# Kernel tuning notes

Hardware: AMD Instinct MI355X
Metric: run time of the kernel (lower is better)

Reference implementation:

```python
import jax, jax.numpy as jnp
import numpy as np

N = 2048          # num nodes == in_channels (f1 = graphs[0].shape[0])
F_IN = 2048       # node feature dim
G1 = 10           # ChebConv out channels
E = 65536         # num edges (avg degree 32)
NUM_CLASSES = 10  # fc1 output


def setup_inputs() -> dict:
    key = jax.random.key(0)
    ks = jax.random.split(key, 6)
    x = jax.random.normal(ks[0], (N, F_IN), dtype=jnp.float32)
    edge_index = jax.random.randint(ks[1], (2, E), 0, N)
    # ChebConv weights: one [F_IN, G1] matrix per Chebyshev order (K=2), glorot-ish init
    s = float(1.0 / np.sqrt(F_IN))
    W0 = jax.random.uniform(ks[2], (F_IN, G1), jnp.float32, -s, s)
    W1 = jax.random.uniform(ks[3], (F_IN, G1), jnp.float32, -s, s)
    b = jnp.zeros((G1,), jnp.float32)
    sf = float(1.0 / np.sqrt(G1))
    Wf = jax.random.uniform(ks[4], (G1, NUM_CLASSES), jnp.float32, -sf, sf)
    bf = jax.random.uniform(ks[5], (NUM_CLASSES,), jnp.float32, -sf, sf)
    return {"x": x, "edge_index": edge_index, "W0": W0, "W1": W1, "b": b, "Wf": Wf, "bf": bf}


def _cheb_edge_weights(edge_index):
    # PyG ChebConv default: sym-normalized Laplacian scaled with lambda_max=2.0.
    # L_hat = 2*L/lambda_max - I = -D^{-1/2} A D^{-1/2}  (zero diagonal).
    row, col = edge_index[0], edge_index[1]
    deg = jax.ops.segment_sum(jnp.ones((E,), jnp.float32), row, num_segments=N)
    dis = jnp.where(deg > 0, jax.lax.rsqrt(jnp.maximum(deg, 1.0)), 0.0)
    return -dis[row] * dis[col]


def reference(x, edge_index, W0, W1, b, Wf, bf):
    row, col = edge_index[0], edge_index[1]
    w = _cheb_edge_weights(edge_index)
    # Tx_0 = x ; Tx_1 = L_hat @ x via gather (source=row) + scatter-add (target=col)
    Tx1 = jax.ops.segment_sum(w[:, None] * x[row], col, num_segments=N)  # [N, F_IN]
    h = x @ W0 + Tx1 @ W1 + b                                            # ChebConv, K=2
    h = jax.nn.relu(h)
    logits = h @ Wf + bf                                                 # fc1
    return jax.nn.log_softmax(logits, axis=1)
```

## Files before the change

### kernel.cpp

```cpp
#include <hip/hip_runtime.h>

#define N_NODES 2048
#define F_IN    2048
#define G1      10
#define NCLS    10
#define NEDGE   65536
#define JCHUNKS 64
#define JPER    32
#define HSLICES 128
#define ZSLICES 64

__device__ float g_p[JCHUNKS * 20 * N_NODES];
__device__ int   g_degp[HSLICES * N_NODES];
__device__ float g_dis[N_NODES];
__device__ float g_y[N_NODES * 20];
__device__ float g_zp[2 * ZSLICES * N_NODES * 5];
__device__ float g_z[N_NODES * G1];

__global__ __launch_bounds__(256) void k_gemm(const float* __restrict__ x,
                                              const float* __restrict__ W0,
                                              const float* __restrict__ W1,
                                              const int* __restrict__ ei) {
    __shared__ float sx[256 * 33];
    int jc      = blockIdx.x;
    int rowbase = blockIdx.y * 256;
    int j0      = jc * JPER;

    #pragma unroll
    for (int rep = 0; rep < 8; ++rep) {
        int idx = rep * 256 + threadIdx.x;
        int r = idx >> 3, c4 = idx & 7;
        float4 v = *(const float4*)(x + (size_t)(rowbase + r) * F_IN + j0 + c4 * 4);
        float* d = sx + r * 33 + c4 * 4;
        d[0] = v.x; d[1] = v.y; d[2] = v.z; d[3] = v.w;
    }
    __syncthreads();

    float acc[20];
    #pragma unroll
    for (int k = 0; k < 20; ++k) acc[k] = 0.f;

    const float* xr = sx + threadIdx.x * 33;
    #pragma unroll
    for (int j = 0; j < JPER; ++j) {
        float xu = xr[j];
        const float* w0r = W0 + (size_t)(j0 + j) * G1;
        const float* w1r = W1 + (size_t)(j0 + j) * G1;
        #pragma unroll
        for (int k = 0; k < G1; ++k) {
            acc[k]      += xu * w0r[k];
            acc[10 + k] += xu * w1r[k];
        }
    }
    int row = rowbase + threadIdx.x;
    #pragma unroll
    for (int k = 0; k < 20; ++k)
        g_p[((size_t)jc * 20 + k) * N_NODES + row] = acc[k];

    if (blockIdx.y < 4) {
        int hs = blockIdx.y * JCHUNKS + jc;
        hs = blockIdx.y * 64 + jc;
        hs = (blockIdx.y << 5) * 2 + jc;
        hs = blockIdx.y * 32 + (jc & 31);
        if (jc < 32) {
            int slice = blockIdx.y * 32 + jc;
            __syncthreads();
            int* h = (int*)sx;
            #pragma unroll
            for (int t = threadIdx.x; t < N_NODES; t += 256) h[t] = 0;
            __syncthreads();
            int base = slice * (NEDGE / HSLICES);
            #pragma unroll
            for (int u = 0; u < 2; ++u)
                atomicAdd(&h[ei[base + u * 256 + threadIdx.x]], 1);
            __syncthreads();
            #pragma unroll
            for (int t = threadIdx.x; t < N_NODES; t += 256)
                g_degp[slice * N_NODES + t] = h[t];
        }
    }
}

__global__ __launch_bounds__(256) void k_reduce() {
    int t   = blockIdx.x * 256 + threadIdx.x;
    int k   = t >> 11;
    int row = t & (N_NODES - 1);
    float s = 0.f;
    #pragma unroll 16
    for (int jc = 0; jc < JCHUNKS; ++jc)
        s += g_p[((size_t)jc * 20 + k) * N_NODES + row];
    g_y[row * 20 + k] = s;
    if (t < N_NODES) {
        int d = 0;
        #pragma unroll 16
        for (int sl = 0; sl < HSLICES; ++sl) d += g_degp[sl * N_NODES + t];
        g_dis[t] = (d > 0) ? rsqrtf((float)d) : 0.f;
    }
}

__global__ __launch_bounds__(256) void k_scatter(const int* __restrict__ ei) {
    __shared__ float zl[N_NODES * 5];
    int khalf  = blockIdx.x >> 6;
    int bslice = blockIdx.x & (ZSLICES - 1);
    float4* zl4 = (float4*)zl;
    #pragma unroll
    for (int t = threadIdx.x; t < N_NODES * 5 / 4; t += 256)
        zl4[t] = make_float4(0.f, 0.f, 0.f, 0.f);
    __syncthreads();
    int base = bslice * (NEDGE / ZSLICES);
    #pragma unroll
    for (int u = 0; u < NEDGE / ZSLICES / 256; ++u) {
        int e = base + u * 256 + threadIdx.x;
        int r = ei[e], c = ei[NEDGE + e];
        float w = -g_dis[r] * g_dis[c];
        const float* y1 = g_y + r * 20 + 10 + khalf * 5;
        float* zz = zl + c * 5;
        #pragma unroll
        for (int kk = 0; kk < 5; ++kk) atomicAdd(&zz[kk], w * y1[kk]);
    }
    __syncthreads();
    float4* dst = (float4*)(g_zp + ((size_t)khalf * ZSLICES + bslice) * (N_NODES * 5));
    #pragma unroll
    for (int t = threadIdx.x; t < N_NODES * 5 / 4; t += 256) dst[t] = zl4[t];
}

__global__ __launch_bounds__(256) void k_zred() {
    int t = blockIdx.x * 256 + threadIdx.x;
    int khalf = t / (N_NODES * 5);
    int rem   = t % (N_NODES * 5);
    float s = 0.f;
    #pragma unroll 16
    for (int sl = 0; sl < ZSLICES; ++sl)
        s += g_zp[((size_t)khalf * ZSLICES + sl) * (N_NODES * 5) + rem];
    int i = rem / 5, kk = rem - i * 5;
    g_z[i * 10 + khalf * 5 + kk] = s;
}

__global__ __launch_bounds__(256) void k_final(const float* __restrict__ b,
                                               const float* __restrict__ Wf,
                                               const float* __restrict__ bfv,
                                               float* __restrict__ out) {
    int i = blockIdx.x * 256 + threadIdx.x;
    float h[G1];
    #pragma unroll
    for (int k = 0; k < G1; ++k)
        h[k] = fmaxf(g_y[i * 20 + k] + g_z[i * 10 + k] + b[k], 0.f);
    float lo[NCLS];
    #pragma unroll
    for (int c = 0; c < NCLS; ++c) lo[c] = bfv[c];
    #pragma unroll
    for (int k = 0; k < G1; ++k) {
        float hk = h[k];
        #pragma unroll
        for (int c = 0; c < NCLS; ++c) lo[c] += hk * Wf[k * NCLS + c];
    }
    float m = lo[0];
    #pragma unroll
    for (int c = 1; c < NCLS; ++c) m = fmaxf(m, lo[c]);
    float s = 0.f;
    #pragma unroll
    for (int c = 0; c < NCLS; ++c) s += expf(lo[c] - m);
    float ls = logf(s);
    #pragma unroll
    for (int c = 0; c < NCLS; ++c) out[i * NCLS + c] = lo[c] - m - ls;
}

extern "C" void kernel_launch(void* const* d_in, const int* in_sizes, int n_in,
                              void* d_out, int out_size, void* d_ws, size_t ws_size,
                              hipStream_t stream) {
    const float* x   = (const float*)d_in[0];
    const int*   ei  = (const int*)d_in[1];
    const float* W0  = (const float*)d_in[2];
    const float* W1  = (const float*)d_in[3];
    const float* b   = (const float*)d_in[4];
    const float* Wf  = (const float*)d_in[5];
    const float* bfv = (const float*)d_in[6];
    float* out = (float*)d_out;

    k_gemm<<<dim3(JCHUNKS, N_NODES / 256), 256, 0, stream>>>(x, W0, W1, ei);
    k_reduce<<<(N_NODES * 20) / 256, 256, 0, stream>>>();
    k_scatter<<<2 * ZSLICES, 256, 0, stream>>>(ei);
    k_zred<<<(N_NODES * G1) / 256, 256, 0, stream>>>();
    k_final<<<N_NODES / 256, 256, 0, stream>>>(b, Wf, bfv, out);
}
```

Before: 111.5 us.

## Fuse all stages into one persistent kernel with software grid barriers

Merges the GEMM, partial reduction, degree count, edge scatter, z reduction and final softmax into a single kernel of 512 blocks separated by atomic grid barriers. The GEMM is retiled to 128 rows by 64 columns with half the block per weight matrix, and degrees are counted with global atomics instead of per-slice histograms. This removes per-launch overhead and intermediate degree partial buffers. It relies on all blocks being co-resident and adds barrier spin cost.

```diff
diff --git a/kernel.cpp b/kernel.cpp
--- a/kernel.cpp
+++ b/kernel.cpp
@@ -5,164 +5,181 @@
 #define G1      10
 #define NCLS    10
 #define NEDGE   65536
-#define JCHUNKS 64
-#define JPER    32
-#define HSLICES 128
-#define ZSLICES 64
+#define JC      32
+#define JPER    64
+#define ROWS    128
+#define ZS      64
+#define GRID    512
+#define BLK     256
 
-__device__ float g_p[JCHUNKS * 20 * N_NODES];
-__device__ int   g_degp[HSLICES * N_NODES];
-__device__ float g_dis[N_NODES];
+__device__ float g_p[JC * 20 * N_NODES];
+__device__ int   g_deg[N_NODES];
 __device__ float g_y[N_NODES * 20];
-__device__ float g_zp[2 * ZSLICES * N_NODES * 5];
+__device__ float g_zp[2 * ZS * N_NODES * 5];
 __device__ float g_z[N_NODES * G1];
 
-__global__ __launch_bounds__(256) void k_gemm(const float* __restrict__ x,
-                                              const float* __restrict__ W0,
-                                              const float* __restrict__ W1,
-                                              const int* __restrict__ ei) {
-    __shared__ float sx[256 * 33];
-    int jc      = blockIdx.x;
-    int rowbase = blockIdx.y * 256;
-    int j0      = jc * JPER;
+__device__ unsigned g_bar_count = 0;
+__device__ unsigned g_bar_gen   = 0;
 
-    #pragma unroll
-    for (int rep = 0; rep < 8; ++rep) {
-        int idx = rep * 256 + threadIdx.x;
-        int r = idx >> 3, c4 = idx & 7;
-        float4 v = *(const float4*)(x + (size_t)(rowbase + r) * F_IN + j0 + c4 * 4);
-        float* d = sx + r * 33 + c4 * 4;
-        d[0] = v.x; d[1] = v.y; d[2] = v.z; d[3] = v.w;
+__device__ __forceinline__ void grid_barrier() {
+    __syncthreads();
+    if (threadIdx.x == 0) {
+        __threadfence();
+        unsigned gen = __hip_atomic_load(&g_bar_gen, __ATOMIC_ACQUIRE,
+                                         __HIP_MEMORY_SCOPE_AGENT);
+        unsigned prev = __hip_atomic_fetch_add(&g_bar_count, 1u, __ATOMIC_ACQ_REL,
+                                               __HIP_MEMORY_SCOPE_AGENT);
+        if (prev == (unsigned)(gridDim.x - 1)) {
+            __hip_atomic_store(&g_bar_count, 0u, __ATOMIC_RELAXED,
+                               __HIP_MEMORY_SCOPE_AGENT);
+            __hip_atomic_fetch_add(&g_bar_gen, 1u, __ATOMIC_RELEASE,
+                                   __HIP_MEMORY_SCOPE_AGENT);
+        } else {
+            while (__hip_atomic_load(&g_bar_gen, __ATOMIC_ACQUIRE,
+                                     __HIP_MEMORY_SCOPE_AGENT) == gen)
+                __builtin_amdgcn_s_sleep(2);
+        }
     }
     __syncthreads();
+}
 
-    float acc[20];
-    #pragma unroll
-    for (int k = 0; k < 20; ++k) acc[k] = 0.f;
+__global__ __launch_bounds__(256, 2) void k_fused(const float* __restrict__ x,
+                                                  const int* __restrict__ ei,
+                                                  const float* __restrict__ W0,
+                                                  const float* __restrict__ W1,
+                                                  const float* __restrict__ b,
+                                                  const float* __restrict__ Wf,
+                                                  const float* __restrict__ bfv,
+                                                  float* __restrict__ out) {
+    __shared__ __align__(16) float smem[N_NODES * 5];
+    const int tid = threadIdx.x;
+    const int bx  = blockIdx.x;
 
-    const float* xr = sx + threadIdx.x * 33;
-    #pragma unroll
-    for (int j = 0; j < JPER; ++j) {
-        float xu = xr[j];
-        const float* w0r = W0 + (size_t)(j0 + j) * G1;
-        const float* w1r = W1 + (size_t)(j0 + j) * G1;
+    {
+        int jc   = bx & (JC - 1);
+        int rb   = bx >> 5;
+        int j0   = jc * JPER;
+        int row0 = rb * ROWS;
         #pragma unroll
-        for (int k = 0; k < G1; ++k) {
-            acc[k]      += xu * w0r[k];
-            acc[10 + k] += xu * w1r[k];
+        for (int rep = 0; rep < 8; ++rep) {
+            int idx = rep * 256 + tid;
+            int r = idx >> 4, c4 = idx & 15;
+            float4 v = *(const float4*)(x + (size_t)(row0 + r) * F_IN + j0 + c4 * 4);
+            float* d = smem + r * 65 + c4 * 4;
+            d[0] = v.x; d[1] = v.y; d[2] = v.z; d[3] = v.w;
+        }
+        if (bx == 0) {
+            #pragma unroll
+            for (int t = tid; t < N_NODES; t += 256) g_deg[t] = 0;
+        }
+        __syncthreads();
+
+        int ri = tid & (ROWS - 1);
+        int kg = tid >> 7;
+        const float* Wm = kg ? W1 : W0;
+        float acc[G1];
+        #pragma unroll
+        for (int k = 0; k < G1; ++k) acc[k] = 0.f;
+        const float* xr = smem + ri * 65;
+        #pragma unroll
+        for (int j = 0; j < JPER; ++j) {
+            float xu = xr[j];
+            const float* wr = Wm + (size_t)(j0 + j) * G1;
+            #pragma unroll
+            for (int k = 0; k < G1; ++k) acc[k] += xu * wr[k];
+        }
+        int row = row0 + ri;
+        #pragma unroll
+        for (int k = 0; k < G1; ++k)
+            g_p[((size_t)jc * 20 + kg * 10 + k) * N_NODES + row] = acc[k];
+    }
+    grid_barrier();
+
+    {
+        int t = bx * 256 + tid;
+        if (t < N_NODES * 20) {
+            int k = t >> 11, row = t & (N_NODES - 1);
+            float s = 0.f;
+            #pragma unroll
+            for (int jc = 0; jc < JC; ++jc)
+                s += g_p[((size_t)jc * 20 + k) * N_NODES + row];
+            g_y[row * 20 + k] = s;
+        } else if (t < N_NODES * 20 + NEDGE) {
+            atomicAdd(&g_deg[ei[t - N_NODES * 20]], 1);
         }
     }
-    int row = rowbase + threadIdx.x;
-    #pragma unroll
-    for (int k = 0; k < 20; ++k)
-        g_p[((size_t)jc * 20 + k) * N_NODES + row] = acc[k];
+    grid_barrier();
 
-    if (blockIdx.y < 4) {
-        int hs = blockIdx.y * JCHUNKS + jc;
-        hs = blockIdx.y * 64 + jc;
-        hs = (blockIdx.y << 5) * 2 + jc;
-        hs = blockIdx.y * 32 + (jc & 31);
-        if (jc < 32) {
-            int slice = blockIdx.y * 32 + jc;
-            __syncthreads();
-            int* h = (int*)sx;
+    if (bx < 2 * ZS) {
+        int khalf = bx >> 6;
+        int slice = bx & (ZS - 1);
+        float4* zl4 = (float4*)smem;
+        #pragma unroll
+        for (int t = tid; t < N_NODES * 5 / 4; t += 256)
+            zl4[t] = make_float4(0.f, 0.f, 0.f, 0.f);
+        __syncthreads();
+        int base = slice * (NEDGE / ZS);
+        #pragma unroll
+        for (int u = 0; u < NEDGE / ZS / 256; ++u) {
+            int e = base + u * 256 + tid;
+            int r = ei[e], c = ei[NEDGE + e];
+            int dr = g_deg[r], dc = g_deg[c];
+            float w = -(dr > 0 ? rsqrtf((float)dr) : 0.f) *
+                       (dc > 0 ? rsqrtf((float)dc) : 0.f);
+            const float* y1 = g_y + r * 20 + 10 + khalf * 5;
+            float* zz = smem + c * 5;
             #pragma unroll
-            for (int t = threadIdx.x; t < N_NODES; t += 256) h[t] = 0;
-            __syncthreads();
-            int base = slice * (NEDGE / HSLICES);
+            for (int kk = 0; kk < 5; ++kk) atomicAdd(&zz[kk], w * y1[kk]);
+        }
+        __syncthreads();
+        float4* dst = (float4*)(g_zp + ((size_t)khalf * ZS + slice) * (N_NODES * 5));
+        #pragma unroll
+        for (int t = tid; t < N_NODES * 5 / 4; t += 256) dst[t] = zl4[t];
+    }
+    grid_barrier();
+
+    {
+        int t = bx * 256 + tid;
+        if (t < N_NODES * G1) {
+            int khalf = t / (N_NODES * 5);
+            int rem   = t % (N_NODES * 5);
+            float s = 0.f;
             #pragma unroll
-            for (int u = 0; u < 2; ++u)
-                atomicAdd(&h[ei[base + u * 256 + threadIdx.x]], 1);
-            __syncthreads();
-            #pragma unroll
-            for (int t = threadIdx.x; t < N_NODES; t += 256)
-                g_degp[slice * N_NODES + t] = h[t];
+            for (int sl = 0; sl < ZS; ++sl)
+                s += g_zp[((size_t)khalf * ZS + sl) * (N_NODES * 5) + rem];
+            int i = rem / 5, kk = rem - i * 5;
+            g_z[i * 10 + khalf * 5 + kk] = s;
         }
     }
-}
+    grid_barrier();
 
-__global__ __launch_bounds__(256) void k_reduce() {
-    int t   = blockIdx.x * 256 + threadIdx.x;
-    int k   = t >> 11;
-    int row = t & (N_NODES - 1);
-    float s = 0.f;
-    #pragma unroll 16
-    for (int jc = 0; jc < JCHUNKS; ++jc)
-        s += g_p[((size_t)jc * 20 + k) * N_NODES + row];
-    g_y[row * 20 + k] = s;
-    if (t < N_NODES) {
-        int d = 0;
-        #pragma unroll 16
-        for (int sl = 0; sl < HSLICES; ++sl) d += g_degp[sl * N_NODES + t];
-        g_dis[t] = (d > 0) ? rsqrtf((float)d) : 0.f;
+    {
+        int i = bx * 256 + tid;
+        if (i < N_NODES) {
+            float h[G1];
+            #pragma unroll
+            for (int k = 0; k < G1; ++k)
+                h[k] = fmaxf(g_y[i * 20 + k] + g_z[i * 10 + k] + b[k], 0.f);
+            float lo[NCLS];
+            #pragma unroll
+            for (int c = 0; c < NCLS; ++c) lo[c] = bfv[c];
+            #pragma unroll
+            for (int k = 0; k < G1; ++k) {
+                float hk = h[k];
+                #pragma unroll
+                for (int c = 0; c < NCLS; ++c) lo[c] += hk * Wf[k * NCLS + c];
+            }
+            float m = lo[0];
+            #pragma unroll
+            for (int c = 1; c < NCLS; ++c) m = fmaxf(m, lo[c]);
+            float s = 0.f;
+            #pragma unroll
+            for (int c = 0; c < NCLS; ++c) s += expf(lo[c] - m);
+            float ls = logf(s);
+            #pragma unroll
+            for (int c = 0; c < NCLS; ++c) out[i * NCLS + c] = lo[c] - m - ls;
+        }
     }
-}
-
-__global__ __launch_bounds__(256) void k_scatter(const int* __restrict__ ei) {
-    __shared__ float zl[N_NODES * 5];
-    int khalf  = blockIdx.x >> 6;
-    int bslice = blockIdx.x & (ZSLICES - 1);
-    float4* zl4 = (float4*)zl;
-    #pragma unroll
-    for (int t = threadIdx.x; t < N_NODES * 5 / 4; t += 256)
-        zl4[t] = make_float4(0.f, 0.f, 0.f, 0.f);
-    __syncthreads();
-    int base = bslice * (NEDGE / ZSLICES);
-    #pragma unroll
-    for (int u = 0; u < NEDGE / ZSLICES / 256; ++u) {
-        int e = base + u * 256 + threadIdx.x;
-        int r = ei[e], c = ei[NEDGE + e];
-        float w = -g_dis[r] * g_dis[c];
-        const float* y1 = g_y + r * 20 + 10 + khalf * 5;
-        float* zz = zl + c * 5;
-        #pragma unroll
-        for (int kk = 0; kk < 5; ++kk) atomicAdd(&zz[kk], w * y1[kk]);
-    }
-    __syncthreads();
-    float4* dst = (float4*)(g_zp + ((size_t)khalf * ZSLICES + bslice) * (N_NODES * 5));
-    #pragma unroll
-    for (int t = threadIdx.x; t < N_NODES * 5 / 4; t += 256) dst[t] = zl4[t];
-}
-
-__global__ __launch_bounds__(256) void k_zred() {
-    int t = blockIdx.x * 256 + threadIdx.x;
-    int khalf = t / (N_NODES * 5);
-    int rem   = t % (N_NODES * 5);
-    float s = 0.f;
-    #pragma unroll 16
-    for (int sl = 0; sl < ZSLICES; ++sl)
-        s += g_zp[((size_t)khalf * ZSLICES + sl) * (N_NODES * 5) + rem];
-    int i = rem / 5, kk = rem - i * 5;
-    g_z[i * 10 + khalf * 5 + kk] = s;
-}
-
-__global__ __launch_bounds__(256) void k_final(const float* __restrict__ b,
-                                               const float* __restrict__ Wf,
-                                               const float* __restrict__ bfv,
-                                               float* __restrict__ out) {
-    int i = blockIdx.x * 256 + threadIdx.x;
-    float h[G1];
-    #pragma unroll
-    for (int k = 0; k < G1; ++k)
-        h[k] = fmaxf(g_y[i * 20 + k] + g_z[i * 10 + k] + b[k], 0.f);
-    float lo[NCLS];
-    #pragma unroll
-    for (int c = 0; c < NCLS; ++c) lo[c] = bfv[c];
-    #pragma unroll
-    for (int k = 0; k < G1; ++k) {
-        float hk = h[k];
-        #pragma unroll
-        for (int c = 0; c < NCLS; ++c) lo[c] += hk * Wf[k * NCLS + c];
-    }
-    float m = lo[0];
-    #pragma unroll
-    for (int c = 1; c < NCLS; ++c) m = fmaxf(m, lo[c]);
-    float s = 0.f;
-    #pragma unroll
-    for (int c = 0; c < NCLS; ++c) s += expf(lo[c] - m);
-    float ls = logf(s);
-    #pragma unroll
-    for (int c = 0; c < NCLS; ++c) out[i * NCLS + c] = lo[c] - m - ls;
 }
 
 extern "C" void kernel_launch(void* const* d_in, const int* in_sizes, int n_in,
@@ -177,9 +194,6 @@
     const float* bfv = (const float*)d_in[6];
     float* out = (float*)d_out;
 
-    k_gemm<<<dim3(JCHUNKS, N_NODES / 256), 256, 0, stream>>>(x, W0, W1, ei);
-    k_reduce<<<(N_NODES * 20) / 256, 256, 0, stream>>>();
-    k_scatter<<<2 * ZSLICES, 256, 0, stream>>>(ei);
-    k_zred<<<(N_NODES * G1) / 256, 256, 0, stream>>>();
-    k_final<<<N_NODES / 256, 256, 0, stream>>>(b, Wf, bfv, out);
+    hipLaunchKernelGGL(k_fused, dim3(GRID), dim3(BLK), 0, stream,
+                       x, ei, W0, W1, b, Wf, bfv, out);
 }
```

After: 398.4 us. 257% more time.
